# Kernel optimization log

Measured on AMD Instinct MI355X. Metric: run time of the kernel, lower is better.

## Reference

```python
import jax, jax.numpy as jnp
import numpy as np

FACTOR = 50
IN_CHANNELS = 512

def setup_inputs() -> dict:
    key = jax.random.key(0)
    ks = jax.random.split(key, 9)
    B, Cin, W, H = 16, 256, 64, 64
    D = 512  # out_channels
    L = W * H
    U = FACTOR * int(np.ceil(np.log(L)))  # 450
    return {
        "input_1": jax.random.normal(ks[0], (B, Cin, W, H), jnp.float32),
        "input_2": jax.random.normal(ks[1], (B, Cin, W, H), jnp.float32),
        "Wq": jax.random.normal(ks[2], (D, 2 * Cin), jnp.float32) * 0.02,
        "bq": jax.random.normal(ks[3], (D,), jnp.float32) * 0.02,
        "Wk": jax.random.normal(ks[4], (D, 2 * Cin), jnp.float32) * 0.02,
        "bk": jax.random.normal(ks[5], (D,), jnp.float32) * 0.02,
        "Wv": jax.random.normal(ks[6], (D, 2 * Cin), jnp.float32) * 0.02,
        "bv": jax.random.normal(ks[7], (D,), jnp.float32) * 0.02,
        "idx_sample": jax.random.randint(ks[8], (U,), 0, L, jnp.int32),
    }

def reference(input_1, input_2, Wq, bq, Wk, bk, Wv, bv, idx_sample):
    x = jnp.concatenate([input_1, input_2], axis=1)  # [B, 2*Cin, W, H]
    B, C, Wd, Ht = x.shape
    L = Wd * Ht
    D = Wq.shape[0]
    # 1x1 convs == per-pixel channel matmul; then torch's raw .view to [B,1,L,D]
    def proj(Wm, bm):
        y = jnp.einsum('bchw,oc->bohw', x, Wm) + bm[None, :, None, None]
        return y.reshape(B, 1, L, D)  # memory reinterpretation, as in torch .view
    q = proj(Wq, bq)
    k = proj(Wk, bk)
    v = proj(Wv, bv)

    u = min(FACTOR * int(np.ceil(np.log(L))), L)  # n_top == sample_k here
    # sampled Q-K scores
    K_sample = k[:, :, idx_sample, :]                      # [B,1,U,D]
    QKs = jnp.einsum('bhld,bhsd->bhls', q, K_sample)       # [B,1,L,U]
    M = QKs.max(-1) - QKs.sum(-1) / L                      # sparsity measure [B,1,L]
    M_top = jax.lax.top_k(M, u)[1]                         # [B,1,u]
    Q_reduce = jnp.take_along_axis(q, M_top[..., None], axis=2)  # [B,1,u,D]
    scores = jnp.einsum('bhud,bhld->bhul', Q_reduce, k)    # [B,1,u,L]
    scores = scores * (1.0 / IN_CHANNELS ** 0.5)

    # initial context: mean of V broadcast over queries
    context = jnp.broadcast_to(v.mean(axis=2, keepdims=True), (B, 1, L, D))
    attn = jax.nn.softmax(scores, axis=-1)                 # [B,1,u,L]
    upd = jnp.einsum('bhul,bhld->bhud', attn, v)           # [B,1,u,D]
    bI = jnp.arange(B)[:, None, None]
    hI = jnp.arange(1)[None, :, None]
    context = context.at[bI, hI, M_top].set(upd)
    # transpose(2,1) then torch .view to [B, D, W, H]
    out = context.transpose(0, 2, 1, 3).reshape(B, D, Wd, Ht)
    return out
```

## Files before the change

kernel.cpp:

```cpp
#include <hip/hip_runtime.h>
#include <cstdint>
#include <cstddef>

#define L_DIM 4096
#define D_DIM 512
#define CIN   256
#define BATCH 16
#define KSPLIT 4
#define CANDMAX 2048
#define CAND_MARGIN 0.06f

typedef _Float16 half8 __attribute__((ext_vector_type(8)));
typedef unsigned short ushort8 __attribute__((ext_vector_type(8)));
typedef float f32x4 __attribute__((ext_vector_type(4)));

__device__ __forceinline__ void gld16(const _Float16* g, _Float16* l) {
    __builtin_amdgcn_global_load_lds(
        (const __attribute__((address_space(1))) unsigned int*)g,
        (__attribute__((address_space(3))) unsigned int*)l,
        16, 0, 0);
}

__global__ __launch_bounds__(256) void convert_w(
    const float* __restrict__ Wq, const float* __restrict__ Wk,
    const float* __restrict__ Wv,
    _Float16* __restrict__ Wh, _Float16* __restrict__ Wl)
{
    const int w = blockIdx.y;
    const float* src = (w == 0) ? Wq : (w == 1) ? Wk : Wv;
    int i = blockIdx.x * 256 + threadIdx.x;
    float xv = src[i];
    _Float16 hi = (_Float16)xv;
    Wh[(size_t)w * 262144 + i] = hi;
    Wl[(size_t)w * 262144 + i] = (_Float16)(xv - (float)hi);
}

__global__ __launch_bounds__(256) void convert_x(
    const float* __restrict__ x1, const float* __restrict__ x2,
    _Float16* __restrict__ XTh, _Float16* __restrict__ XTl, int phase)
{
    const int bb = blockIdx.z;
    const int b = phase * 8 + bb;
    const int s0 = blockIdx.x * 64;
    const int c0 = blockIdx.y * 64;
    __shared__ float t[64][65];
    const int tid = threadIdx.x;
    const int g = tid >> 6, sy = tid & 63;
    const float* src = (c0 < CIN)
        ? (x1 + (size_t)b * CIN * L_DIM + (size_t)c0 * L_DIM)
        : (x2 + (size_t)b * CIN * L_DIM + (size_t)(c0 - CIN) * L_DIM);
    #pragma unroll
    for (int r = 0; r < 16; r++) {
        int cl = g * 16 + r;
        t[cl][sy] = src[(size_t)cl * L_DIM + s0 + sy];
    }
    __syncthreads();
    _Float16* outh = XTh + (size_t)bb * L_DIM * 512 + (size_t)s0 * 512 + c0;
    _Float16* outl = XTl + (size_t)bb * L_DIM * 512 + (size_t)s0 * 512 + c0;
    #pragma unroll
    for (int r = 0; r < 16; r++) {
        int sl = g * 16 + r;
        float xv = t[sy][sl];
        _Float16 hi = (_Float16)xv;
        float lo = xv - (float)hi;
        outh[(size_t)sl * 512 + sy] = hi;
        outl[(size_t)sl * 512 + sy] = (_Float16)lo;
    }
}

__global__ __launch_bounds__(256) void proj_mfma_qk(
    const _Float16* __restrict__ Wh, const _Float16* __restrict__ Wl,
    const _Float16* __restrict__ XTh, const _Float16* __restrict__ XTl,
    const float* __restrict__ bq, const float* __restrict__ bk,
    _Float16* __restrict__ qh, _Float16* __restrict__ ql,
    _Float16* __restrict__ kh, _Float16* __restrict__ kl,
    int phase)
{
    const int z = blockIdx.z;
    const int bb = z >> 1, w = z & 1;
    const int b = phase * 8 + bb;
    const _Float16* Ah_g = Wh + (size_t)w * 262144;
    const _Float16* Al_g = Wl + (size_t)w * 262144;
    const _Float16* Bh_g = XTh + (size_t)bb * ((size_t)L_DIM * 512);
    const _Float16* Bl_g = XTl + (size_t)bb * ((size_t)L_DIM * 512);
    const float* bias = (w == 0) ? bq : bk;
    _Float16* outh = ((w == 0) ? qh : kh) + (size_t)b * ((size_t)D_DIM * L_DIM);
    _Float16* outl = ((w == 0) ? ql : kl) + (size_t)b * ((size_t)D_DIM * L_DIM);

    const int m0 = blockIdx.y * 128;
    const int n0 = blockIdx.x * 128;

    __shared__ _Float16 lds[4 * 128 * 32];
    _Float16* ldsA_h = lds;
    _Float16* ldsA_l = lds + 4096;
    _Float16* ldsB_h = lds + 8192;
    _Float16* ldsB_l = lds + 12288;

    const int tid = threadIdx.x;
    const int w4 = tid >> 6, lane = tid & 63;
    const int lr = lane & 15, quad = lane >> 4;
    const int wr = w4 >> 1, wc = w4 & 1;

    f32x4 acc[4][4] = {};

    const int q1 = w4 * 128 + lane, q2 = q1 + 64;
    const int r1 = q1 >> 2, c41 = (q1 & 3) ^ ((r1 >> 1) & 3);
    const int r2 = q2 >> 2, c42 = (q2 & 3) ^ ((r2 >> 1) & 3);

    const _Float16* pAh1 = Ah_g + (size_t)(m0 + r1) * 512 + c41 * 8;
    const _Float16* pAh2 = Ah_g + (size_t)(m0 + r2) * 512 + c42 * 8;
    const _Float16* pAl1 = Al_g + (size_t)(m0 + r1) * 512 + c41 * 8;
    const _Float16* pAl2 = Al_g + (size_t)(m0 + r2) * 512 + c42 * 8;
    const _Float16* pBh1 = Bh_g + (size_t)(n0 + r1) * 512 + c41 * 8;
    const _Float16* pBh2 = Bh_g + (size_t)(n0 + r2) * 512 + c42 * 8;
    const _Float16* pBl1 = Bl_g + (size_t)(n0 + r1) * 512 + c41 * 8;
    const _Float16* pBl2 = Bl_g + (size_t)(n0 + r2) * 512 + c42 * 8;

    _Float16* d1 = (_Float16*)(lds) + (size_t)(w4 * 128) * 8;
    _Float16* d2 = (_Float16*)(lds) + (size_t)(w4 * 128 + 64) * 8;

    const int qsw = (quad ^ ((lr >> 1) & 3)) * 8;

    for (int k0 = 0; k0 < 512; k0 += 32) {
        if (k0) __syncthreads();
        gld16(pAh1 + k0, d1);
        gld16(pAh2 + k0, d2);
        gld16(pAl1 + k0, d1 + 4096);
        gld16(pAl2 + k0, d2 + 4096);
        gld16(pBh1 + k0, d1 + 8192);
        gld16(pBh2 + k0, d2 + 8192);
        gld16(pBl1 + k0, d1 + 12288);
        gld16(pBl2 + k0, d2 + 12288);
        __syncthreads();

        half8 fAh[4], fAl[4];
        #pragma unroll
        for (int i = 0; i < 4; i++) {
            int m = wr * 64 + i * 16 + lr;
            fAh[i] = *(const half8*)(ldsA_h + m * 32 + qsw);
            fAl[i] = *(const half8*)(ldsA_l + m * 32 + qsw);
        }
        #pragma unroll
        for (int j = 0; j < 4; j++) {
            int n = wc * 64 + j * 16 + lr;
            half8 fBh = *(const half8*)(ldsB_h + n * 32 + qsw);
            half8 fBl = *(const half8*)(ldsB_l + n * 32 + qsw);
            #pragma unroll
            for (int i = 0; i < 4; i++) {
                acc[i][j] = __builtin_amdgcn_mfma_f32_16x16x32_f16(fAh[i], fBh, acc[i][j], 0, 0, 0);
                acc[i][j] = __builtin_amdgcn_mfma_f32_16x16x32_f16(fAl[i], fBh, acc[i][j], 0, 0, 0);
                acc[i][j] = __builtin_amdgcn_mfma_f32_16x16x32_f16(fAh[i], fBl, acc[i][j], 0, 0, 0);
            }
        }
    }

    #pragma unroll
    for (int i = 0; i < 4; i++) {
        int mg = m0 + wr * 64 + i * 16 + quad * 4;
        #pragma unroll
        for (int r = 0; r < 4; r++) {
            float bvv = bias[mg + r];
            #pragma unroll
            for (int j = 0; j < 4; j++) {
                int ng = n0 + wc * 64 + j * 16 + lr;
                float val = acc[i][j][r] + bvv;
                _Float16 hi = (_Float16)val;
                size_t off = (size_t)(mg + r) * L_DIM + ng;
                outh[off] = hi;
                outl[off] = (_Float16)(val - (float)hi);
            }
        }
    }
}

__global__ __launch_bounds__(256) void proj_mfma_v(
    const _Float16* __restrict__ Wh, const _Float16* __restrict__ XTh,
    const float* __restrict__ bv, _Float16* __restrict__ vh, int phase)
{
    const int bb = blockIdx.z;
    const int b = phase * 8 + bb;
    const _Float16* Ah_g = Wh + (size_t)2 * 262144;
    const _Float16* Bh_g = XTh + (size_t)bb * ((size_t)L_DIM * 512);
    _Float16* outh = vh + (size_t)b * ((size_t)D_DIM * L_DIM);

    const int m0 = blockIdx.y * 128;
    const int n0 = blockIdx.x * 128;

    __shared__ _Float16 lds[2 * 128 * 32];
    _Float16* ldsA_h = lds;
    _Float16* ldsB_h = lds + 4096;

    const int tid = threadIdx.x;
    const int w4 = tid >> 6, lane = tid & 63;
    const int lr = lane & 15, quad = lane >> 4;
    const int wr = w4 >> 1, wc = w4 & 1;

    f32x4 acc[4][4] = {};

    const int q1 = w4 * 128 + lane, q2 = q1 + 64;
    const int r1 = q1 >> 2, c41 = (q1 & 3) ^ ((r1 >> 1) & 3);
    const int r2 = q2 >> 2, c42 = (q2 & 3) ^ ((r2 >> 1) & 3);

    const _Float16* pAh1 = Ah_g + (size_t)(m0 + r1) * 512 + c41 * 8;
    const _Float16* pAh2 = Ah_g + (size_t)(m0 + r2) * 512 + c42 * 8;
    const _Float16* pBh1 = Bh_g + (size_t)(n0 + r1) * 512 + c41 * 8;
    const _Float16* pBh2 = Bh_g + (size_t)(n0 + r2) * 512 + c42 * 8;

    _Float16* d1 = (_Float16*)(lds) + (size_t)(w4 * 128) * 8;
    _Float16* d2 = (_Float16*)(lds) + (size_t)(w4 * 128 + 64) * 8;

    const int qsw = (quad ^ ((lr >> 1) & 3)) * 8;

    for (int k0 = 0; k0 < 512; k0 += 32) {
        if (k0) __syncthreads();
        gld16(pAh1 + k0, d1);
        gld16(pAh2 + k0, d2);
        gld16(pBh1 + k0, d1 + 4096);
        gld16(pBh2 + k0, d2 + 4096);
        __syncthreads();

        half8 fAh[4];
        #pragma unroll
        for (int i = 0; i < 4; i++) {
            int m = wr * 64 + i * 16 + lr;
            fAh[i] = *(const half8*)(ldsA_h + m * 32 + qsw);
        }
        #pragma unroll
        for (int j = 0; j < 4; j++) {
            int n = wc * 64 + j * 16 + lr;
            half8 fBh = *(const half8*)(ldsB_h + n * 32 + qsw);
            #pragma unroll
            for (int i = 0; i < 4; i++)
                acc[i][j] = __builtin_amdgcn_mfma_f32_16x16x32_f16(fAh[i], fBh, acc[i][j], 0, 0, 0);
        }
    }

    #pragma unroll
    for (int i = 0; i < 4; i++) {
        int mg = m0 + wr * 64 + i * 16 + quad * 4;
        #pragma unroll
        for (int r = 0; r < 4; r++) {
            float bvv = bv[mg + r];
            #pragma unroll
            for (int j = 0; j < 4; j++) {
                int ng = n0 + wc * 64 + j * 16 + lr;
                outh[(size_t)(mg + r) * L_DIM + ng] = (_Float16)(acc[i][j][r] + bvv);
            }
        }
    }
}

__global__ __launch_bounds__(256) void qks_x1(
    const _Float16* __restrict__ qh, const _Float16* __restrict__ kh,
    const int* __restrict__ idx_sample,
    float* __restrict__ Mmax, float* __restrict__ Msum, int U, int nst)
{
    const int b = blockIdx.z;
    const int stile = blockIdx.y;
    const int l0 = blockIdx.x * 128;
    const int s0 = stile * 128;
    const size_t perB = (size_t)D_DIM * L_DIM;
    const _Float16* qh_b = qh + (size_t)b * perB;
    const _Float16* kh_b = kh + (size_t)b * perB;

    __shared__ _Float16 ldsAh[4096];
    __shared__ _Float16 ldsBh[4096];
    __shared__ int sidx[128];
    __shared__ float redm[8][128];
    __shared__ float reds[8][128];

    const int tid = threadIdx.x;
    const int w4 = tid >> 6, lane = tid & 63;
    const int lr = lane & 15, quad = lane >> 4;
    const int ws = w4 >> 1, wl = w4 & 1;

    if (tid < 128) {
        int s = s0 + tid;
        sidx[tid] = (s < U) ? idx_sample[s] : idx_sample[0];
    }
    __syncthreads();

    f32x4 acc[4][4] = {};
    const int qsw = (quad ^ ((lr >> 1) & 3)) * 8;

    for (int k0 = 0; k0 < 512; k0 += 32) {
        #pragma unroll
        for (int t = 0; t < 2; t++) {
            int c = w4 * 128 + t * 64 + lane;
            int row = c >> 2, part = (c & 3) ^ ((row >> 1) & 3);
            int krow = sidx[row];
            size_t go = (size_t)krow * 512 + k0 + part * 8;
            size_t qo = (size_t)(l0 + row) * 512 + k0 + part * 8;
            int base = (w4 * 128 + t * 64) * 8;
            gld16(kh_b + go, ldsAh + base);
            gld16(qh_b + qo, ldsBh + base);
        }
        __syncthreads();

        half8 fAh[4];
        #pragma unroll
        for (int i = 0; i < 4; i++) {
            int s = ws * 64 + i * 16 + lr;
            fAh[i] = *(const half8*)(ldsAh + s * 32 + qsw);
        }
        #pragma unroll
        for (int j = 0; j < 4; j++) {
            int l = wl * 64 + j * 16 + lr;
            half8 fBh = *(const half8*)(ldsBh + l * 32 + qsw);
            #pragma unroll
            for (int i = 0; i < 4; i++)
                acc[i][j] = __builtin_amdgcn_mfma_f32_16x16x32_f16(fAh[i], fBh, acc[i][j], 0, 0, 0);
        }
        __syncthreads();
    }

    float runmax[4], runsum[4];
    #pragma unroll
    for (int j = 0; j < 4; j++) { runmax[j] = -__builtin_inff(); runsum[j] = 0.f; }
    #pragma unroll
    for (int i = 0; i < 4; i++) {
        #pragma unroll
        for (int r = 0; r < 4; r++) {
            int sg = s0 + ws * 64 + i * 16 + quad * 4 + r;
            if (sg < U) {
                #pragma unroll
                for (int j = 0; j < 4; j++) {
                    runmax[j] = fmaxf(runmax[j], acc[i][j][r]);
                    runsum[j] += acc[i][j][r];
                }
            }
        }
    }
    #pragma unroll
    for (int j = 0; j < 4; j++) {
        int l = wl * 64 + j * 16 + lr;
        redm[ws * 4 + quad][l] = runmax[j];
        reds[ws * 4 + quad][l] = runsum[j];
    }
    __syncthreads();
    if (tid < 128) {
        float gm = -__builtin_inff(), gs = 0.f;
        #pragma unroll
        for (int t = 0; t < 8; t++) { gm = fmaxf(gm, redm[t][tid]); gs += reds[t][tid]; }
        size_t o = ((size_t)b * nst + stile) * L_DIM + l0 + tid;
        Mmax[o] = gm;
        Msum[o] = gs;
    }
}

__global__ __launch_bounds__(512) void topk_cand(
    const float* __restrict__ Mmax, const float* __restrict__ Msum,
    int* __restrict__ candlist, int* __restrict__ ncand, int U, int nst)
{
    const int b = blockIdx.x;
    const int tid = threadIdx.x;
    __shared__ int wcnt[8];
    __shared__ int basec;

    float Mv[8];
    unsigned mykey[8];
    #pragma unroll
    for (int t = 0; t < 8; t++) {
        int l = t * 512 + tid;
        float gm = -__builtin_inff(), gs = 0.f;
        for (int st = 0; st < nst; st++) {
            size_t o = ((size_t)b * nst + st) * L_DIM + l;
            gm = fmaxf(gm, Mmax[o]);
            gs += Msum[o];
        }
        float M = gm - gs * (1.f / (float)L_DIM);
        Mv[t] = M;
        unsigned bits = __float_as_uint(M);
        mykey[t] = (bits & 0x80000000u) ? ~bits : (bits | 0x80000000u);
    }
    if (tid == 0) basec = 0;

    const int wv = tid >> 6, lane = tid & 63;
    unsigned lo = 0u, hi = 0xFFFFFFFFu;
    while (lo < hi) {
        unsigned hl = hi - lo;
        unsigned mid = lo + (hl >> 1) + (hl & 1u);
        int c = 0;
        #pragma unroll
        for (int t = 0; t < 8; t++) c += (mykey[t] >= mid) ? 1 : 0;
        #pragma unroll
        for (int o = 32; o > 0; o >>= 1) c += __shfl_down(c, o, 64);
        if (lane == 0) wcnt[wv] = c;
        __syncthreads();
        int total = 0;
        #pragma unroll
        for (int i = 0; i < 8; i++) total += wcnt[i];
        if (total >= U) lo = mid; else hi = mid - 1;
        __syncthreads();
    }
    unsigned tb = (lo & 0x80000000u) ? (lo & 0x7FFFFFFFu) : ~lo;
    float Tval = __uint_as_float(tb) - CAND_MARGIN;
    #pragma unroll
    for (int t = 0; t < 8; t++) {
        if (Mv[t] >= Tval) {
            int pos = atomicAdd(&basec, 1);
            if (pos < CANDMAX) candlist[b * CANDMAX + pos] = t * 512 + tid;
        }
    }
    __syncthreads();
    if (tid == 0) ncand[b] = (basec < CANDMAX) ? basec : CANDMAX;
}

__global__ __launch_bounds__(256) void refine_mfma(
    const _Float16* __restrict__ qh, const _Float16* __restrict__ ql,
    const _Float16* __restrict__ kh, const _Float16* __restrict__ kl,
    const int* __restrict__ idx_sample, const int* __restrict__ candlist,
    const int* __restrict__ ncand,
    float* __restrict__ Rmax, float* __restrict__ Rsum, int U, int nst)
{
    const int b = blockIdx.z;
    const int nc = ncand[b];
    const int c0 = blockIdx.x * 128;
    if (c0 >= nc) return;
    const int stile = blockIdx.y;
    const int s0 = stile * 128;
    const size_t perB = (size_t)D_DIM * L_DIM;
    const _Float16* qh_b = qh + (size_t)b * perB;
    const _Float16* ql_b = ql + (size_t)b * perB;
    const _Float16* kh_b = kh + (size_t)b * perB;
    const _Float16* kl_b = kl + (size_t)b * perB;

    __shared__ _Float16 ldsAh[4096], ldsAl[4096];
    __shared__ _Float16 ldsBh[4096], ldsBl[4096];
    __shared__ int sidx[128];
    __shared__ int crow[128];
    __shared__ float redm[8][128];
    __shared__ float reds[8][128];

    const int tid = threadIdx.x;
    const int w4 = tid >> 6, lane = tid & 63;
    const int lr = lane & 15, quad = lane >> 4;
    const int ws = w4 >> 1, wl = w4 & 1;

    if (tid < 128) {
        int s = s0 + tid;
        sidx[tid] = (s < U) ? idx_sample[s] : idx_sample[0];
        int c = c0 + tid;
        crow[tid] = candlist[b * CANDMAX + (c < nc ? c : 0)];
    }
    __syncthreads();

    f32x4 acc[4][4] = {};
    const int qsw = (quad ^ ((lr >> 1) & 3)) * 8;

    for (int k0 = 0; k0 < 512; k0 += 32) {
        #pragma unroll
        for (int t = 0; t < 2; t++) {
            int c = w4 * 128 + t * 64 + lane;
            int row = c >> 2, part = (c & 3) ^ ((row >> 1) & 3);
            int krow = sidx[row];
            size_t go = (size_t)krow * 512 + k0 + part * 8;
            size_t qo = (size_t)crow[row] * 512 + k0 + part * 8;
            int base = (w4 * 128 + t * 64) * 8;
            gld16(kh_b + go, ldsAh + base);
            gld16(kl_b + go, ldsAl + base);
            gld16(qh_b + qo, ldsBh + base);
            gld16(ql_b + qo, ldsBl + base);
        }
        __syncthreads();

        half8 fAh[4], fAl[4];
        #pragma unroll
        for (int i = 0; i < 4; i++) {
            int s = ws * 64 + i * 16 + lr;
            fAh[i] = *(const half8*)(ldsAh + s * 32 + qsw);
            fAl[i] = *(const half8*)(ldsAl + s * 32 + qsw);
        }
        #pragma unroll
        for (int j = 0; j < 4; j++) {
            int l = wl * 64 + j * 16 + lr;
            half8 fBh = *(const half8*)(ldsBh + l * 32 + qsw);
            half8 fBl = *(const half8*)(ldsBl + l * 32 + qsw);
            #pragma unroll
            for (int i = 0; i < 4; i++) {
                acc[i][j] = __builtin_amdgcn_mfma_f32_16x16x32_f16(fAh[i], fBh, acc[i][j], 0, 0, 0);
                acc[i][j] = __builtin_amdgcn_mfma_f32_16x16x32_f16(fAl[i], fBh, acc[i][j], 0, 0, 0);
                acc[i][j] = __builtin_amdgcn_mfma_f32_16x16x32_f16(fAh[i], fBl, acc[i][j], 0, 0, 0);
            }
        }
        __syncthreads();
    }

    float runmax[4], runsum[4];
    #pragma unroll
    for (int j = 0; j < 4; j++) { runmax[j] = -__builtin_inff(); runsum[j] = 0.f; }
    #pragma unroll
    for (int i = 0; i < 4; i++) {
        #pragma unroll
        for (int r = 0; r < 4; r++) {
            int sg = s0 + ws * 64 + i * 16 + quad * 4 + r;
            if (sg < U) {
                #pragma unroll
                for (int j = 0; j < 4; j++) {
                    runmax[j] = fmaxf(runmax[j], acc[i][j][r]);
                    runsum[j] += acc[i][j][r];
                }
            }
        }
    }
    #pragma unroll
    for (int j = 0; j < 4; j++) {
        int l = wl * 64 + j * 16 + lr;
        redm[ws * 4 + quad][l] = runmax[j];
        reds[ws * 4 + quad][l] = runsum[j];
    }
    __syncthreads();
    if (tid < 128) {
        float gm = -__builtin_inff(), gs = 0.f;
        #pragma unroll
        for (int t = 0; t < 8; t++) { gm = fmaxf(gm, redm[t][tid]); gs += reds[t][tid]; }
        size_t o = ((size_t)b * nst + stile) * CANDMAX + c0 + tid;
        Rmax[o] = gm;
        Rsum[o] = gs;
    }
}

__global__ __launch_bounds__(512) void topk_final(
    const float* __restrict__ Rmax, const float* __restrict__ Rsum,
    const int* __restrict__ candlist, const int* __restrict__ ncand,
    int* __restrict__ topidx, int U, int nst)
{
    const int b = blockIdx.x;
    const int tid = threadIdx.x;
    __shared__ int wcnt[8];
    __shared__ int basec;
    const int nc = ncand[b];

    unsigned mykey[4];
    #pragma unroll
    for (int t = 0; t < 4; t++) {
        int c = t * 512 + tid;
        float M = -__builtin_inff();
        if (c < nc) {
            float gm = -__builtin_inff(), gs = 0.f;
            for (int st = 0; st < nst; st++) {
                size_t o = ((size_t)b * nst + st) * CANDMAX + c;
                gm = fmaxf(gm, Rmax[o]);
                gs += Rsum[o];
            }
            M = gm - gs * (1.f / (float)L_DIM);
        }
        unsigned bits = __float_as_uint(M);
        mykey[t] = (bits & 0x80000000u) ? ~bits : (bits | 0x80000000u);
    }
    if (tid == 0) basec = 0;

    const int wv = tid >> 6, lane = tid & 63;
    unsigned lo = 0u, hi = 0xFFFFFFFFu;
    while (lo < hi) {
        unsigned hl = hi - lo;
        unsigned mid = lo + (hl >> 1) + (hl & 1u);
        int c = 0;
        #pragma unroll
        for (int t = 0; t < 4; t++) c += (mykey[t] >= mid) ? 1 : 0;
        #pragma unroll
        for (int o = 32; o > 0; o >>= 1) c += __shfl_down(c, o, 64);
        if (lane == 0) wcnt[wv] = c;
        __syncthreads();
        int total = 0;
        #pragma unroll
        for (int i = 0; i < 8; i++) total += wcnt[i];
        if (total >= U) lo = mid; else hi = mid - 1;
        __syncthreads();
    }
    #pragma unroll
    for (int t = 0; t < 4; t++) {
        if (mykey[t] >= lo) {
            int pos = atomicAdd(&basec, 1);
            if (pos < U) topidx[b * U + pos] = candlist[b * CANDMAX + t * 512 + tid];
        }
    }
}

__global__ __launch_bounds__(512) void vmean_partial(
    const _Float16* __restrict__ vh, float* __restrict__ partial)
{
    const int ch = blockIdx.x, b = blockIdx.y;
    const int d = threadIdx.x;
    const _Float16* vhb = vh + (size_t)b * ((size_t)D_DIM * L_DIM);
    float acc = 0.f;
    const int lbeg = ch * 128;
    for (int l = lbeg; l < lbeg + 128; l++)
        acc += (float)vhb[(size_t)l * D_DIM + d];
    partial[((size_t)b * 32 + ch) * D_DIM + d] = acc;
}

__global__ __launch_bounds__(512) void vmean_reduce(const float* __restrict__ partial,
                                                    float* __restrict__ vmean)
{
    const int b = blockIdx.x;
    const int d = threadIdx.x;
    float acc = 0.f;
    for (int ch = 0; ch < 32; ch++) acc += partial[((size_t)b * 32 + ch) * D_DIM + d];
    vmean[b * D_DIM + d] = acc * (1.f / (float)L_DIM);
}

__global__ __launch_bounds__(256) void fill_out(const float* __restrict__ vmean,
                                                float* __restrict__ out)
{
    const int z = blockIdx.x;
    const int b = z >> 6, lch = z & 63;
    __shared__ float vm[512];
    vm[threadIdx.x] = vmean[b * 512 + threadIdx.x];
    vm[threadIdx.x + 256] = vmean[b * 512 + threadIdx.x + 256];
    __syncthreads();
    float* op = out + (size_t)b * ((size_t)D_DIM * L_DIM) + (size_t)lch * 64 * 512;
    #pragma unroll
    for (int it = 0; it < 32; it++) {
        int flat = (threadIdx.x + it * 256) * 4;
        int d = flat & 511;
        float4 r = { vm[d], vm[d + 1], vm[d + 2], vm[d + 3] };
        *(float4*)&op[flat] = r;
    }
}

__global__ __launch_bounds__(256) void zero_sel(const int* __restrict__ topidx,
                                                float* __restrict__ out, int U)
{
    const int u = blockIdx.x, b = blockIdx.y;
    int row = topidx[b * U + u];
    float2 z = { 0.f, 0.f };
    *(float2*)&out[(size_t)b * ((size_t)D_DIM * L_DIM) + (size_t)row * 512
                   + threadIdx.x * 2] = z;
}

__global__ __launch_bounds__(256) void scores_mfma(
    const _Float16* __restrict__ qh, const _Float16* __restrict__ kh,
    const int* __restrict__ topidx,
    _Float16* __restrict__ sh, int U)
{
    const int b = blockIdx.z;
    const int s0 = blockIdx.x * 128;
    const int u0 = blockIdx.y * 128;
    const size_t perB = (size_t)D_DIM * L_DIM;
    const _Float16* qh_b = qh + (size_t)b * perB;
    const _Float16* kh_b = kh + (size_t)b * perB;
    _Float16* sh_b = sh + (size_t)b * (size_t)U * L_DIM;

    __shared__ _Float16 ldsAh[4096];
    __shared__ _Float16 ldsBh[4096];
    __shared__ int arow[128];

    const int tid = threadIdx.x;
    const int w4 = tid >> 6, lane = tid & 63;
    const int lr = lane & 15, quad = lane >> 4;
    const int wu = w4 >> 1, wn = w4 & 1;

    if (tid < 128) {
        int u = u0 + tid;
        arow[tid] = topidx[b * U + (u < U ? u : U - 1)];
    }
    __syncthreads();

    f32x4 acc[4][4] = {};
    const int qsw = (quad ^ ((lr >> 1) & 3)) * 8;

    for (int k0 = 0; k0 < 512; k0 += 32) {
        #pragma unroll
        for (int t = 0; t < 2; t++) {
            int c = w4 * 128 + t * 64 + lane;
            int row = c >> 2, part = (c & 3) ^ ((row >> 1) & 3);
            size_t go = (size_t)arow[row] * 512 + k0 + part * 8;
            size_t ko = (size_t)(s0 + row) * 512 + k0 + part * 8;
            int base = (w4 * 128 + t * 64) * 8;
            gld16(qh_b + go, ldsAh + base);
            gld16(kh_b + ko, ldsBh + base);
        }
        __syncthreads();

        half8 fAh[4];
        #pragma unroll
        for (int i = 0; i < 4; i++) {
            int u = wu * 64 + i * 16 + lr;
            fAh[i] = *(const half8*)(ldsAh + u * 32 + qsw);
        }
        #pragma unroll
        for (int j = 0; j < 4; j++) {
            int s = wn * 64 + j * 16 + lr;
            half8 fBh = *(const half8*)(ldsBh + s * 32 + qsw);
            #pragma unroll
            for (int i = 0; i < 4; i++)
                acc[i][j] = __builtin_amdgcn_mfma_f32_16x16x32_f16(fAh[i], fBh, acc[i][j], 0, 0, 0);
        }
        __syncthreads();
    }

    const float scale = 0.044194173824159216f;
    #pragma unroll
    for (int i = 0; i < 4; i++) {
        #pragma unroll
        for (int r = 0; r < 4; r++) {
            int u = u0 + wu * 64 + i * 16 + quad * 4 + r;
            if (u < U) {
                #pragma unroll
                for (int j = 0; j < 4; j++) {
                    int s = s0 + wn * 64 + j * 16 + lr;
                    sh_b[(size_t)u * L_DIM + s] = (_Float16)(acc[i][j][r] * scale);
                }
            }
        }
    }
}

__global__ __launch_bounds__(256) void softmax_h(_Float16* __restrict__ sh)
{
    _Float16* hrow = sh + (size_t)blockIdx.x * L_DIM;
    const int tid = threadIdx.x;
    float x[16];
    #pragma unroll
    for (int t = 0; t < 2; t++) {
        half8 h8 = *(const half8*)(hrow + tid * 8 + t * 2048);
        #pragma unroll
        for (int i = 0; i < 8; i++) x[t * 8 + i] = (float)h8[i];
    }
    __shared__ float red[256];
    float lm = -__builtin_inff();
    #pragma unroll
    for (int i = 0; i < 16; i++) lm = fmaxf(lm, x[i]);
    red[tid] = lm;
    __syncthreads();
    for (int o = 128; o > 0; o >>= 1) {
        if (tid < o) red[tid] = fmaxf(red[tid], red[tid + o]);
        __syncthreads();
    }
    float m = red[0];
    __syncthreads();
    float ls = 0.f;
    #pragma unroll
    for (int i = 0; i < 16; i++) { x[i] = __expf(x[i] - m); ls += x[i]; }
    red[tid] = ls;
    __syncthreads();
    for (int o = 128; o > 0; o >>= 1) {
        if (tid < o) red[tid] += red[tid + o];
        __syncthreads();
    }
    float inv = 1.f / red[0];
    #pragma unroll
    for (int t = 0; t < 2; t++) {
        half8 h8;
        #pragma unroll
        for (int i = 0; i < 8; i++) h8[i] = (_Float16)(x[t * 8 + i] * inv);
        *(half8*)(hrow + tid * 8 + t * 2048) = h8;
    }
}

__global__ __launch_bounds__(256) void upd_mfma(
    const _Float16* __restrict__ sh, const _Float16* __restrict__ vh,
    const int* __restrict__ topidx, float* __restrict__ out, int U)
{
    const int zz = blockIdx.z;
    const int b = zz >> 2, ks = zz & 3;
    const int n0 = blockIdx.y * 128;
    const int u0 = blockIdx.x * 128;
    const size_t perB = (size_t)D_DIM * L_DIM;
    const _Float16* ah_b = sh + (size_t)b * (size_t)U * L_DIM;
    const _Float16* vh_b = vh + (size_t)b * perB;

    __shared__ _Float16 ldsAh[4096];
    __shared__ _Float16 ldsBh[4096];

    const int tid = threadIdx.x;
    const int w4 = tid >> 6, lane = tid & 63;
    const int lr = lane & 15, quad = lane >> 4;
    const int wu = w4 >> 1, wd = w4 & 1;

    const int part = tid & 15, spair = tid >> 4;
    const int s_b = spair * 2;
    const int colw = ((spair >> 2) + part) & 3;
    const int so2 = (s_b & 7);

    f32x4 acc[4][4] = {};
    const int qsw = (quad ^ ((lr >> 1) & 3)) * 8;

    const int kbeg = ks * (L_DIM / KSPLIT);
    const int kend = kbeg + (L_DIM / KSPLIT);
    for (int k0 = kbeg; k0 < kend; k0 += 32) {
        #pragma unroll
        for (int t = 0; t < 2; t++) {
            int c = w4 * 128 + t * 64 + lane;
            int u = c >> 2, pt = (c & 3) ^ ((u >> 1) & 3);
            int urow = u0 + u; if (urow >= U) urow = U - 1;
            size_t ao = (size_t)urow * L_DIM + k0 + pt * 8;
            int base = (w4 * 128 + t * 64) * 8;
            gld16(ah_b + ao, ldsAh + base);
        }
        {
            const _Float16* s0p = vh_b + (size_t)(k0 + s_b) * 512 + n0 + part * 8;
            const _Float16* s1p = s0p + 512;
            ushort8 a0 = *(const ushort8*)s0p;
            ushort8 a1 = *(const ushort8*)s1p;
            #pragma unroll
            for (int t = 0; t < 8; t++) {
                int dd = part * 8 + t;
                unsigned int ph = (unsigned int)a0[t] | ((unsigned int)a1[t] << 16);
                *(unsigned int*)(ldsBh + dd * 32 + colw * 8 + so2) = ph;
            }
        }
        __syncthreads();

        half8 fAh[4];
        #pragma unroll
        for (int i = 0; i < 4; i++) {
            int u = wu * 64 + i * 16 + lr;
            fAh[i] = *(const half8*)(ldsAh + u * 32 + qsw);
        }
        #pragma unroll
        for (int j = 0; j < 4; j++) {
            int dd = wd * 64 + j * 16 + lr;
            int col = (quad + (dd >> 3)) & 3;
            half8 fBh = *(const half8*)(ldsBh + dd * 32 + col * 8);
            #pragma unroll
            for (int i = 0; i < 4; i++)
                acc[i][j] = __builtin_amdgcn_mfma_f32_16x16x32_f16(fAh[i], fBh, acc[i][j], 0, 0, 0);
        }
        __syncthreads();
    }

    #pragma unroll
    for (int i = 0; i < 4; i++) {
        #pragma unroll
        for (int r = 0; r < 4; r++) {
            int u = u0 + wu * 64 + i * 16 + quad * 4 + r;
            if (u < U) {
                int lrow = topidx[b * U + u];
                #pragma unroll
                for (int j = 0; j < 4; j++) {
                    int dd = n0 + wd * 64 + j * 16 + lr;
                    unsafeAtomicAdd(&out[(size_t)b * perB + (size_t)lrow * 512 + dd],
                                    acc[i][j][r]);
                }
            }
        }
    }
}

extern "C" void kernel_launch(void* const* d_in, const int* in_sizes, int n_in,
                              void* d_out, int out_size, void* d_ws, size_t ws_size,
                              hipStream_t stream)
{
    const float* x1 = (const float*)d_in[0];
    const float* x2 = (const float*)d_in[1];
    const float* Wq = (const float*)d_in[2];
    const float* bq = (const float*)d_in[3];
    const float* Wk = (const float*)d_in[4];
    const float* bk = (const float*)d_in[5];
    const float* Wv = (const float*)d_in[6];
    const float* bv = (const float*)d_in[7];
    const int*  idx = (const int*)d_in[8];
    const int U = in_sizes[8];
    const int nst = (U + 127) / 128;

    float* out = (float*)d_out;

    const size_t perB = (size_t)D_DIM * L_DIM;
    const size_t tenH = (size_t)BATCH * perB;
    _Float16* qh = (_Float16*)d_ws;
    _Float16* ql = qh + tenH;
    _Float16* kh = ql + tenH;
    _Float16* kl = kh + tenH;
    _Float16* vh = kl + tenH;
    float* S = (float*)(vh + tenH);

    _Float16* XTh = (_Float16*)S;
    _Float16* XTl = XTh + (size_t)8 * L_DIM * 512;
    _Float16* Wh  = XTl + (size_t)8 * L_DIM * 512;
    _Float16* Wl  = Wh + (size_t)3 * 512 * 512;

    _Float16* sh = (_Float16*)S;
    float* vmean = (float*)(sh + (size_t)BATCH * (size_t)U * L_DIM);
    float* partU = vmean + (size_t)BATCH * D_DIM;
    float* vpart = partU;
    float* Mmax  = partU;
    float* Msum  = Mmax + (size_t)BATCH * nst * L_DIM;
    int* topidx   = (int*)(Msum + (size_t)BATCH * nst * L_DIM);
    int* candlist = topidx + BATCH * 512;
    int* ncand    = candlist + BATCH * CANDMAX;
    float* Rmax   = (float*)(ncand + 64);
    float* Rsum   = Rmax + (size_t)BATCH * nst * CANDMAX;

    convert_w<<<dim3(1024, 3), 256, 0, stream>>>(Wq, Wk, Wv, Wh, Wl);

    for (int phase = 0; phase < 2; phase++) {
        convert_x<<<dim3(64, 8, 8), 256, 0, stream>>>(x1, x2, XTh, XTl, phase);
        proj_mfma_qk<<<dim3(L_DIM / 128, D_DIM / 128, 8 * 2), 256, 0, stream>>>(
            Wh, Wl, XTh, XTl, bq, bk, qh, ql, kh, kl, phase);
        proj_mfma_v<<<dim3(L_DIM / 128, D_DIM / 128, 8), 256, 0, stream>>>(
            Wh, XTh, bv, vh, phase);
    }

    vmean_partial<<<dim3(32, BATCH), 512, 0, stream>>>(vh, vpart);
    vmean_reduce<<<BATCH, 512, 0, stream>>>(vpart, vmean);
    fill_out<<<BATCH * 64, 256, 0, stream>>>(vmean, out);

    qks_x1<<<dim3(L_DIM / 128, nst, BATCH), 256, 0, stream>>>(
        qh, kh, idx, Mmax, Msum, U, nst);
    topk_cand<<<BATCH, 512, 0, stream>>>(Mmax, Msum, candlist, ncand, U, nst);
    refine_mfma<<<dim3(CANDMAX / 128, nst, BATCH), 256, 0, stream>>>(
        qh, ql, kh, kl, idx, candlist, ncand, Rmax, Rsum, U, nst);
    topk_final<<<BATCH, 512, 0, stream>>>(Rmax, Rsum, candlist, ncand, topidx, U, nst);

    const int utiles = (U + 127) / 128;
    scores_mfma<<<dim3(L_DIM / 128, utiles, BATCH), 256, 0, stream>>>(
        qh, kh, topidx, sh, U);
    softmax_h<<<BATCH * U, 256, 0, stream>>>(sh);
    zero_sel<<<dim3(U, BATCH), 256, 0, stream>>>(topidx, out, U);
    upd_mfma<<<dim3(utiles, D_DIM / 128, BATCH * KSPLIT), 256, 0, stream>>>(
        sh, vh, topidx, out, U);
}
```

Measured before the change: 913.9 us.

## Rewrite QK projection GEMM with 256x256 tiles and triple-buffered async loads

```diff
diff --git a/kernel.cpp b/kernel.cpp
--- a/kernel.cpp
+++ b/kernel.cpp
@@ -68,7 +68,7 @@
     }
 }
 
-__global__ __launch_bounds__(256) void proj_mfma_qk(
+__global__ __launch_bounds__(512, 2) void proj_qk_pipe(
     const _Float16* __restrict__ Wh, const _Float16* __restrict__ Wl,
     const _Float16* __restrict__ XTh, const _Float16* __restrict__ XTl,
     const float* __restrict__ bq, const float* __restrict__ bk,
@@ -87,76 +87,81 @@
     _Float16* outh = ((w == 0) ? qh : kh) + (size_t)b * ((size_t)D_DIM * L_DIM);
     _Float16* outl = ((w == 0) ? ql : kl) + (size_t)b * ((size_t)D_DIM * L_DIM);
 
-    const int m0 = blockIdx.y * 128;
-    const int n0 = blockIdx.x * 128;
-
-    __shared__ _Float16 lds[4 * 128 * 32];
-    _Float16* ldsA_h = lds;
-    _Float16* ldsA_l = lds + 4096;
-    _Float16* ldsB_h = lds + 8192;
-    _Float16* ldsB_l = lds + 12288;
+    const int m0 = blockIdx.y * 256;
+    const int n0 = blockIdx.x * 256;
+
+    __shared__ _Float16 lds[3 * 16384];
 
     const int tid = threadIdx.x;
-    const int w4 = tid >> 6, lane = tid & 63;
+    const int lane = tid & 63;
+    const int w8 = tid >> 6;
     const int lr = lane & 15, quad = lane >> 4;
-    const int wr = w4 >> 1, wc = w4 & 1;
-
-    f32x4 acc[4][4] = {};
-
-    const int q1 = w4 * 128 + lane, q2 = q1 + 64;
-    const int r1 = q1 >> 2, c41 = (q1 & 3) ^ ((r1 >> 1) & 3);
-    const int r2 = q2 >> 2, c42 = (q2 & 3) ^ ((r2 >> 1) & 3);
-
-    const _Float16* pAh1 = Ah_g + (size_t)(m0 + r1) * 512 + c41 * 8;
-    const _Float16* pAh2 = Ah_g + (size_t)(m0 + r2) * 512 + c42 * 8;
-    const _Float16* pAl1 = Al_g + (size_t)(m0 + r1) * 512 + c41 * 8;
-    const _Float16* pAl2 = Al_g + (size_t)(m0 + r2) * 512 + c42 * 8;
-    const _Float16* pBh1 = Bh_g + (size_t)(n0 + r1) * 512 + c41 * 8;
-    const _Float16* pBh2 = Bh_g + (size_t)(n0 + r2) * 512 + c42 * 8;
-    const _Float16* pBl1 = Bl_g + (size_t)(n0 + r1) * 512 + c41 * 8;
-    const _Float16* pBl2 = Bl_g + (size_t)(n0 + r2) * 512 + c42 * 8;
-
-    _Float16* d1 = (_Float16*)(lds) + (size_t)(w4 * 128) * 8;
-    _Float16* d2 = (_Float16*)(lds) + (size_t)(w4 * 128 + 64) * 8;
-
+    const int wr = w8 >> 2, wc = w8 & 3;
     const int qsw = (quad ^ ((lr >> 1) & 3)) * 8;
 
-    for (int k0 = 0; k0 < 512; k0 += 32) {
-        if (k0) __syncthreads();
-        gld16(pAh1 + k0, d1);
-        gld16(pAh2 + k0, d2);
-        gld16(pAl1 + k0, d1 + 4096);
-        gld16(pAl2 + k0, d2 + 4096);
-        gld16(pBh1 + k0, d1 + 8192);
-        gld16(pBh2 + k0, d2 + 8192);
-        gld16(pBl1 + k0, d1 + 12288);
-        gld16(pBl2 + k0, d2 + 12288);
-        __syncthreads();
-
-        half8 fAh[4], fAl[4];
-        #pragma unroll
-        for (int i = 0; i < 4; i++) {
-            int m = wr * 64 + i * 16 + lr;
-            fAh[i] = *(const half8*)(ldsA_h + m * 32 + qsw);
-            fAl[i] = *(const half8*)(ldsA_l + m * 32 + qsw);
-        }
-        #pragma unroll
-        for (int j = 0; j < 4; j++) {
-            int n = wc * 64 + j * 16 + lr;
-            half8 fBh = *(const half8*)(ldsB_h + n * 32 + qsw);
-            half8 fBl = *(const half8*)(ldsB_l + n * 32 + qsw);
+    const int q0 = tid, q1 = tid + 512;
+    const int r0 = q0 >> 2, s0_ = ((q0 & 3) ^ ((r0 >> 1) & 3)) * 8;
+    const int r1 = q1 >> 2, s1_ = ((q1 & 3) ^ ((r1 >> 1) & 3)) * 8;
+    const size_t a0off = (size_t)(m0 + r0) * 512 + s0_;
+    const size_t a1off = (size_t)(m0 + r1) * 512 + s1_;
+    const size_t b0off = (size_t)(n0 + r0) * 512 + s0_;
+    const size_t b1off = (size_t)(n0 + r1) * 512 + s1_;
+
+    f32x4 acc[8][4] = {};
+
+#define STAGE(tt)                                                         \
+    {                                                                     \
+        const int pc_ = (tt) >> 4;                                        \
+        const int kk_ = ((tt) & 15) * 32;                                 \
+        const _Float16* As_ = (pc_ == 1) ? Al_g : Ah_g;                   \
+        const _Float16* Bs_ = (pc_ == 2) ? Bl_g : Bh_g;                   \
+        _Float16* dst_ = lds + ((tt) % 3) * 16384;                        \
+        gld16(As_ + a0off + kk_, dst_ + q0 * 8);                          \
+        gld16(As_ + a1off + kk_, dst_ + q1 * 8);                          \
+        gld16(Bs_ + b0off + kk_, dst_ + 8192 + q0 * 8);                   \
+        gld16(Bs_ + b1off + kk_, dst_ + 8192 + q1 * 8);                   \
+    }
+
+    STAGE(0);
+    STAGE(1);
+
+    const int NT = 48;
+    for (int kt = 0; kt < NT; kt++) {
+        if (kt + 2 < NT) STAGE(kt + 2);
+        if (kt + 2 < NT)      asm volatile("s_waitcnt vmcnt(8)" ::: "memory");
+        else if (kt + 1 < NT) asm volatile("s_waitcnt vmcnt(4)" ::: "memory");
+        else                  asm volatile("s_waitcnt vmcnt(0)" ::: "memory");
+        __builtin_amdgcn_sched_barrier(0);
+        __builtin_amdgcn_s_barrier();
+        __builtin_amdgcn_sched_barrier(0);
+
+        const _Float16* bufA = lds + (kt % 3) * 16384;
+        const _Float16* bufB = bufA + 8192;
+        half8 fA[8], fB[4];
+        #pragma unroll
+        for (int i = 0; i < 8; i++)
+            fA[i] = *(const half8*)(bufA + (wr * 128 + i * 16 + lr) * 32 + qsw);
+        #pragma unroll
+        for (int j = 0; j < 4; j++)
+            fB[j] = *(const half8*)(bufB + (wc * 64 + j * 16 + lr) * 32 + qsw);
+
+        __builtin_amdgcn_s_setprio(1);
+        #pragma unroll
+        for (int j = 0; j < 4; j++)
             #pragma unroll
-            for (int i = 0; i < 4; i++) {
-                acc[i][j] = __builtin_amdgcn_mfma_f32_16x16x32_f16(fAh[i], fBh, acc[i][j], 0, 0, 0);
-                acc[i][j] = __builtin_amdgcn_mfma_f32_16x16x32_f16(fAl[i], fBh, acc[i][j], 0, 0, 0);
-                acc[i][j] = __builtin_amdgcn_mfma_f32_16x16x32_f16(fAh[i], fBl, acc[i][j], 0, 0, 0);
-            }
-        }
-    }
-
-    #pragma unroll
-    for (int i = 0; i < 4; i++) {
-        int mg = m0 + wr * 64 + i * 16 + quad * 4;
+            for (int i = 0; i < 8; i++)
+                acc[i][j] = __builtin_amdgcn_mfma_f32_16x16x32_f16(fA[i], fB[j], acc[i][j], 0, 0, 0);
+        __builtin_amdgcn_s_setprio(0);
+
+        __builtin_amdgcn_sched_barrier(0);
+        __builtin_amdgcn_s_barrier();
+        __builtin_amdgcn_sched_barrier(0);
+    }
+#undef STAGE
+
+    #pragma unroll
+    for (int i = 0; i < 8; i++) {
+        int mg = m0 + wr * 128 + i * 16 + quad * 4;
         #pragma unroll
         for (int r = 0; r < 4; r++) {
             float bvv = bias[mg + r];
@@ -887,7 +892,7 @@
 
     for (int phase = 0; phase < 2; phase++) {
         convert_x<<<dim3(64, 8, 8), 256, 0, stream>>>(x1, x2, XTh, XTl, phase);
-        proj_mfma_qk<<<dim3(L_DIM / 128, D_DIM / 128, 8 * 2), 256, 0, stream>>>(
+        proj_qk_pipe<<<dim3(L_DIM / 256, D_DIM / 256, 8 * 2), 512, 0, stream>>>(
             Wh, Wl, XTh, XTl, bq, bk, qh, ql, kh, kl, phase);
         proj_mfma_v<<<dim3(L_DIM / 128, D_DIM / 128, 8), 256, 0, stream>>>(
             Wh, XTh, bv, vh, phase);
```

Result: no change. 928.9 us (+1.6%).
